# Kernel tuning notes

Hardware: AMD Instinct MI355X
Metric: run time of the kernel (lower is better)

## Reference

```python
import jax, jax.numpy as jnp
import numpy as np

EPS = 1e-6  # annotated-transformer LayerNorm eps


def setup_inputs() -> dict:
    key = jax.random.key(0)
    ks = jax.random.split(key, 6)
    B, S, D, F, G_dom = 32, 512, 1024, 2048, 4
    x = jax.random.normal(ks[0], (B, S, D), dtype=jnp.float32)
    # disjoint partition of the batch into 4 equal domain groups (like the
    # per-domain LongTensor index lists in the torch forward)
    perm = jax.random.permutation(ks[1], B).astype(jnp.int32)
    idx = perm.reshape(G_dom, B // G_dom)  # [4, 8]
    s1 = 1.0 / np.sqrt(D)
    s2 = 1.0 / np.sqrt(F)
    W1 = jax.random.normal(ks[2], (G_dom, D, F), dtype=jnp.float32) * s1
    B1 = jnp.zeros((G_dom, F), dtype=jnp.float32)
    W2 = jax.random.normal(ks[3], (G_dom, F, D), dtype=jnp.float32) * s2
    B2 = jnp.zeros((G_dom, D), dtype=jnp.float32)
    G = jnp.ones((G_dom, D), dtype=jnp.float32)
    Bn = jnp.zeros((G_dom, D), dtype=jnp.float32)
    return {"x": x, "idx": idx, "W1": W1, "B1": B1, "W2": W2, "B2": B2,
            "G": G, "Bn": Bn}


def _layer_norm(x, g, b):
    # matches torch: a_2 * (x - mean) / (std + eps) + b_2, std unbiased (ddof=1)
    mu = jnp.mean(x, axis=-1, keepdims=True)
    sd = jnp.std(x, axis=-1, keepdims=True, ddof=1)
    return g * (x - mu) / (sd + EPS) + b


def reference(x, idx, W1, B1, W2, B2, G, Bn):
    # gather per-domain token groups: [n_dom, per_dom, S, D]
    xg = x[idx]
    # SublayerConnection (eval mode, dropout off): x + adapter(norm(x))
    h = _layer_norm(xg, G[:, None, None, :], Bn[:, None, None, :])
    h = jax.nn.relu(jnp.einsum('gbsd,gdf->gbsf', h, W1) + B1[:, None, None, :])
    a = jnp.einsum('gbsf,gfd->gbsd', h, W2) + B2[:, None, None, :]
    out_g = xg + a
    # scatter combine (index_copy): indices are a disjoint partition
    S_, D_ = x.shape[1], x.shape[2]
    out = jnp.zeros_like(x).at[idx.reshape(-1)].set(out_g.reshape(-1, S_, D_))
    return out
```

## Files before the change

kernel.cpp:

```cpp
#include <hip/hip_runtime.h>
#include <hip/hip_bf16.h>


#define S_DIM 512
#define D_DIM 1024
#define F_DIM 2048
#define MPG   4096

typedef __attribute__((ext_vector_type(8))) short  short8;
typedef __attribute__((ext_vector_type(4))) float  f32x4;

__device__ __forceinline__ void gll16(const void* g, void* l) {
  __builtin_amdgcn_global_load_lds((__attribute__((address_space(1))) void*)g,
                                   (__attribute__((address_space(3))) void*)l,
                                   16, 0, 0);
}
#define VMC2()  asm volatile("s_waitcnt vmcnt(2)" ::: "memory")
#define VMC4()  asm volatile("s_waitcnt vmcnt(4)" ::: "memory")
#define SB()    __builtin_amdgcn_sched_barrier(0)
#define BAR()   __builtin_amdgcn_s_barrier()

__global__ __launch_bounds__(256) void transpose_cast_kernel(
    const float* __restrict__ W1, const float* __restrict__ W2,
    __hip_bfloat16* __restrict__ W1t, __hip_bfloat16* __restrict__ W2t)
{
  __shared__ float tl[32][33];
  const int bid = blockIdx.x;
  const float* src; __hip_bfloat16* dst;
  int R, C, tr, tc;
  if (bid < 8192) {
    const int g = bid >> 11, t = bid & 2047;
    R = 1024; C = 2048; tr = t >> 6; tc = t & 63;
    src = W1 + (size_t)g * R * C;
    dst = W1t + (size_t)g * R * C;
  } else {
    const int b2 = bid - 8192;
    const int g = b2 >> 11, t = b2 & 2047;
    R = 2048; C = 1024; tr = t >> 5; tc = t & 31;
    src = W2 + (size_t)g * R * C;
    dst = W2t + (size_t)g * R * C;
  }
  const int tx = threadIdx.x & 31, ty = threadIdx.x >> 5;
  const int r0 = tr * 32, c0 = tc * 32;
#pragma unroll
  for (int i = 0; i < 4; ++i)
    tl[ty + 8 * i][tx] = src[(size_t)(r0 + ty + 8 * i) * C + (c0 + tx)];
  __syncthreads();
#pragma unroll
  for (int i = 0; i < 4; ++i)
    dst[(size_t)(c0 + ty + 8 * i) * R + (r0 + tx)] = __float2bfloat16(tl[tx][ty + 8 * i]);
}

__global__ __launch_bounds__(256) void ln_gather_kernel(
    const float* __restrict__ x, const int* __restrict__ idx,
    const float* __restrict__ G, const float* __restrict__ Bn,
    __hip_bfloat16* __restrict__ Xn)
{
  const int wid  = (blockIdx.x * 256 + threadIdx.x) >> 6;
  const int lane = threadIdx.x & 63;
  const int g = wid >> 12;
  const int r = wid & 4095;
  const int j = r >> 9;
  const int tok = r & 511;
  const int b = idx[g * 8 + j];

  const float* src = x + ((size_t)b * S_DIM + tok) * D_DIM + lane * 16;
  float4 vq[4];
#pragma unroll
  for (int i = 0; i < 4; ++i) vq[i] = ((const float4*)src)[i];
  const float* va = (const float*)vq;

  float s = 0.f, s2 = 0.f;
#pragma unroll
  for (int i = 0; i < 16; ++i) { s += va[i]; s2 += va[i] * va[i]; }
#pragma unroll
  for (int o = 32; o > 0; o >>= 1) { s += __shfl_xor(s, o); s2 += __shfl_xor(s2, o); }

  const float mu  = s * (1.0f / 1024.0f);
  float var = fmaxf(s2 * (1.0f / 1024.0f) - mu * mu, 0.0f) * (1024.0f / 1023.0f);
  const float rs  = 1.0f / (sqrtf(var) + 1e-6f);

  float4 gq[4], bq[4];
  const float* gp = G  + (size_t)g * D_DIM + lane * 16;
  const float* bp = Bn + (size_t)g * D_DIM + lane * 16;
#pragma unroll
  for (int i = 0; i < 4; ++i) { gq[i] = ((const float4*)gp)[i]; bq[i] = ((const float4*)bp)[i]; }
  const float* ga = (const float*)gq;
  const float* be = (const float*)bq;

  __align__(16) __hip_bfloat16 ob[16];
#pragma unroll
  for (int i = 0; i < 16; ++i)
    ob[i] = __float2bfloat16(ga[i] * (va[i] - mu) * rs + be[i]);

  __hip_bfloat16* dst = Xn + ((size_t)g * MPG + r) * D_DIM + lane * 16;
  ((uint4*)dst)[0] = *(const uint4*)&ob[0];
  ((uint4*)dst)[1] = *(const uint4*)&ob[8];
}

template <bool SECOND>
__global__ __launch_bounds__(512, 2) void gemm_kernel(
    const __hip_bfloat16* __restrict__ A,
    const __hip_bfloat16* __restrict__ Bw,
    const float* __restrict__ bias,
    const float* __restrict__ xres,
    const int* __restrict__ idx,
    __hip_bfloat16* __restrict__ obf,
    float* __restrict__ of32,
    const int N, const int K, const int NT)
{
  extern __shared__ char lds[];
  const int ntile = N >> 8;
  const int nwg = gridDim.x;
  const int bid0 = blockIdx.x;
  const int bid = (bid0 & 7) * (nwg >> 3) + (bid0 >> 3);
  const int mt = bid / ntile, nt = bid % ntile;
  const int g  = mt >> 4;
  const int tid = threadIdx.x;
  const int w = tid >> 6, lane = tid & 63;
  const int wm = w >> 2, wn = w & 3;

  const __hip_bfloat16* Ab = A + (size_t)mt * 256 * K;
  const __hip_bfloat16* Bb = Bw + ((size_t)g * N + (size_t)nt * 256) * K;

  const int sp   = (lane & 7) ^ ((lane >> 3) & 7);
  const int srow = 2 * (lane >> 3) + (sp >> 2);
  const int skof = (sp & 3) * 8;
  const __hip_bfloat16* Ag0 = Ab + (size_t)(w * 32 + srow) * K + skof;
  const __hip_bfloat16* Ag1 = Ag0 + (size_t)16 * K;
  const __hip_bfloat16* Bg0 = Bb + (size_t)(w * 32 + srow) * K + skof;
  const __hip_bfloat16* Bg1 = Bg0 + (size_t)16 * K;

  const int l15 = lane & 15, sl = lane >> 4;
  const int slot_phys = (((l15 & 1) << 2) + sl) ^ ((l15 >> 1) & 7);
  const int lane_c = ((l15 >> 1) << 7) + (slot_phys << 4);

  f32x4 acc[8][4] = {};
  short8 frA0[4], frA1[4], frB0[4], frB1[4];

#define STAGE(BUFX, MAT, KH, TN) {                                          \
    const int koff = (TN) * 64 + (KH) * 32;                                 \
    char* d = lds + (BUFX) + ((KH) * 2 + (MAT)) * 16384 + w * 2048;         \
    if (MAT) { gll16(Bg0 + koff, d); gll16(Bg1 + koff, d + 1024); }         \
    else     { gll16(Ag0 + koff, d); gll16(Ag1 + koff, d + 1024); } }

#define RDA(DST, BUFX, KH, MH) {                                            \
    const char* base_ = lds + (BUFX) + (KH) * 32768 + wm * 8192 +           \
                        (MH) * 4096 + lane_c;                               \
    _Pragma("unroll") for (int mm = 0; mm < 4; ++mm)                        \
      DST[mm] = *(const short8*)(base_ + mm * 1024); }

#define RDB(DST, BUFX, KH) {                                                \
    const char* base_ = lds + (BUFX) + 16384 + (KH) * 32768 + wn * 4096 +   \
                        lane_c;                                             \
    _Pragma("unroll") for (int n = 0; n < 4; ++n)                           \
      DST[n] = *(const short8*)(base_ + n * 1024); }

#define MF(MH, FA, FB) {                                                    \
    __builtin_amdgcn_s_setprio(1);                                          \
    _Pragma("unroll") for (int mm = 0; mm < 4; ++mm)                        \
      _Pragma("unroll") for (int n = 0; n < 4; ++n)                         \
        acc[(MH) * 4 + mm][n] = __builtin_amdgcn_mfma_f32_16x16x32_bf16(    \
            FA[mm], FB[n], acc[(MH) * 4 + mm][n], 0, 0, 0);                 \
    __builtin_amdgcn_s_setprio(0); }

  STAGE(0, 0, 0, 0); STAGE(0, 1, 0, 0); STAGE(0, 0, 1, 0); STAGE(0, 1, 1, 0);
  VMC4();
  BAR();
  RDA(frA0, 0, 0, 0);
  RDB(frB0, 0, 0);

  for (int t = 0; t < NT; ++t) {
    const int bufb = (t & 1) << 16;
    const int bufx = bufb ^ 65536;
    const int tn = (t + 1 == NT) ? 0 : t + 1;
    SB(); BAR(); SB();
    RDA(frA1, bufb, 0, 1);
    STAGE(bufx, 0, 0, tn);
    SB();
    MF(0, frA0, frB0);
    SB(); VMC2(); BAR(); SB();
    RDA(frA0, bufb, 1, 0);
    RDB(frB1, bufb, 1);
    STAGE(bufx, 1, 0, tn);
    SB();
    MF(1, frA1, frB0);
    SB(); BAR(); SB();
    RDA(frA1, bufb, 1, 1);
    STAGE(bufx, 0, 1, tn);
    SB();
    MF(0, frA0, frB1);
    SB(); VMC2(); BAR(); SB();
    RDA(frA0, bufx, 0, 0);
    RDB(frB0, bufx, 0);
    STAGE(bufx, 1, 1, tn);
    SB();
    MF(1, frA1, frB1);
  }
#undef STAGE
#undef RDA
#undef RDB
#undef MF

  const int cc  = lane & 15;
  const int cr4 = (lane >> 4) * 4;

  float bv[4];
#pragma unroll
  for (int n = 0; n < 4; ++n)
    bv[n] = bias[(size_t)g * N + nt * 256 + wn * 64 + n * 16 + cc];

  if constexpr (!SECOND) {
#pragma unroll
    for (int m = 0; m < 8; ++m) {
      const int grow0 = mt * 256 + wm * 128 + m * 16 + cr4;
#pragma unroll
      for (int n = 0; n < 4; ++n) {
        const int gcol = nt * 256 + wn * 64 + n * 16 + cc;
#pragma unroll
        for (int i = 0; i < 4; ++i) {
          const float v = fmaxf(acc[m][n][i] + bv[n], 0.0f);
          obf[(size_t)(grow0 + i) * N + gcol] = __float2bfloat16(v);
        }
      }
    }
  } else {
    const int rbase = (mt & 15) * 256;
    const int b = idx[g * 8 + (rbase >> 9)];
    const size_t ob = (size_t)b * S_DIM * D_DIM;
#pragma unroll
    for (int m = 0; m < 8; ++m) {
      const int rloc = rbase + wm * 128 + m * 16 + cr4;
#pragma unroll
      for (int n = 0; n < 4; ++n) {
        const int gcol = nt * 256 + wn * 64 + n * 16 + cc;
#pragma unroll
        for (int i = 0; i < 4; ++i) {
          const int tok = (rloc + i) & 511;
          const size_t off = ob + (size_t)tok * D_DIM + gcol;
          of32[off] = acc[m][n][i] + bv[n] + xres[off];
        }
      }
    }
  }
}

extern "C" void kernel_launch(void* const* d_in, const int* in_sizes, int n_in,
                              void* d_out, int out_size, void* d_ws, size_t ws_size,
                              hipStream_t stream) {
  const float* x  = (const float*)d_in[0];
  const int*   idx = (const int*)d_in[1];
  const float* W1 = (const float*)d_in[2];
  const float* B1 = (const float*)d_in[3];
  const float* W2 = (const float*)d_in[4];
  const float* B2 = (const float*)d_in[5];
  const float* G  = (const float*)d_in[6];
  const float* Bn = (const float*)d_in[7];
  float* out = (float*)d_out;

  char* ws = (char*)d_ws;
  __hip_bfloat16* Xn  = (__hip_bfloat16*)(ws);
  __hip_bfloat16* W1t = (__hip_bfloat16*)(ws + 33554432);
  __hip_bfloat16* W2t = (__hip_bfloat16*)(ws + 50331648);
  __hip_bfloat16* H1  = (__hip_bfloat16*)(ws + 67108864);

  (void)hipFuncSetAttribute((const void*)gemm_kernel<false>,
                            hipFuncAttributeMaxDynamicSharedMemorySize, 131072);
  (void)hipFuncSetAttribute((const void*)gemm_kernel<true>,
                            hipFuncAttributeMaxDynamicSharedMemorySize, 131072);

  transpose_cast_kernel<<<dim3(16384), dim3(256), 0, stream>>>(W1, W2, W1t, W2t);
  ln_gather_kernel<<<dim3(4096), dim3(256), 0, stream>>>(x, idx, G, Bn, Xn);
  gemm_kernel<false><<<dim3(512), dim3(512), 131072, stream>>>(
      Xn, W1t, B1, nullptr, nullptr, H1, nullptr, F_DIM, D_DIM, 16);
  gemm_kernel<true><<<dim3(256), dim3(512), 131072, stream>>>(
      H1, W2t, B2, x, idx, nullptr, out, D_DIM, F_DIM, 32);
}
```

Measured before the change: 197.6 us.

## Replace double-buffered register fragments with single set and explicit LDS waits

Drops the ping-pong register fragments (frA0/frA1/frB0/frB1) for a single frA/frB set. Each MFMA block now waits on lgkmcnt(0) and barriers before and after, so LDS reads no longer overlap the previous block's MFMAs. This cuts VGPR pressure, which could allow higher occupancy. The cost is more barriers and serialized LDS-read/compute phases within a wave.

```diff
diff --git a/kernel.cpp b/kernel.cpp
--- a/kernel.cpp
+++ b/kernel.cpp
@@ -15,8 +15,8 @@
                                    (__attribute__((address_space(3))) void*)l,
                                    16, 0, 0);
 }
-#define VMC2()  asm volatile("s_waitcnt vmcnt(2)" ::: "memory")
 #define VMC4()  asm volatile("s_waitcnt vmcnt(4)" ::: "memory")
+#define LGKM0() asm volatile("s_waitcnt lgkmcnt(0)" ::: "memory")
 #define SB()    __builtin_amdgcn_sched_barrier(0)
 #define BAR()   __builtin_amdgcn_s_barrier()
 
@@ -136,7 +136,7 @@
   const int lane_c = ((l15 >> 1) << 7) + (slot_phys << 4);
 
   f32x4 acc[8][4] = {};
-  short8 frA0[4], frA1[4], frB0[4], frB1[4];
+  short8 frA[4], frB[4];
 
 #define STAGE(BUFX, MAT, KH, TN) {                                          \
     const int koff = (TN) * 64 + (KH) * 32;                                 \
@@ -144,58 +144,56 @@
     if (MAT) { gll16(Bg0 + koff, d); gll16(Bg1 + koff, d + 1024); }         \
     else     { gll16(Ag0 + koff, d); gll16(Ag1 + koff, d + 1024); } }
 
-#define RDA(DST, BUFX, KH, MH) {                                            \
+#define RDA(BUFX, KH, MH) {                                                 \
     const char* base_ = lds + (BUFX) + (KH) * 32768 + wm * 8192 +           \
                         (MH) * 4096 + lane_c;                               \
     _Pragma("unroll") for (int mm = 0; mm < 4; ++mm)                        \
-      DST[mm] = *(const short8*)(base_ + mm * 1024); }
-
-#define RDB(DST, BUFX, KH) {                                                \
+      frA[mm] = *(const short8*)(base_ + mm * 1024); }
+
+#define RDB(BUFX, KH) {                                                     \
     const char* base_ = lds + (BUFX) + 16384 + (KH) * 32768 + wn * 4096 +   \
                         lane_c;                                             \
     _Pragma("unroll") for (int n = 0; n < 4; ++n)                           \
-      DST[n] = *(const short8*)(base_ + n * 1024); }
-
-#define MF(MH, FA, FB) {                                                    \
+      frB[n] = *(const short8*)(base_ + n * 1024); }
+
+#define MF(MH) {                                                            \
     __builtin_amdgcn_s_setprio(1);                                          \
     _Pragma("unroll") for (int mm = 0; mm < 4; ++mm)                        \
       _Pragma("unroll") for (int n = 0; n < 4; ++n)                         \
         acc[(MH) * 4 + mm][n] = __builtin_amdgcn_mfma_f32_16x16x32_bf16(    \
-            FA[mm], FB[n], acc[(MH) * 4 + mm][n], 0, 0, 0);                 \
+            frA[mm], frB[n], acc[(MH) * 4 + mm][n], 0, 0, 0);               \
     __builtin_amdgcn_s_setprio(0); }
 
   STAGE(0, 0, 0, 0); STAGE(0, 1, 0, 0); STAGE(0, 0, 1, 0); STAGE(0, 1, 1, 0);
   VMC4();
   BAR();
-  RDA(frA0, 0, 0, 0);
-  RDB(frB0, 0, 0);
 
   for (int t = 0; t < NT; ++t) {
     const int bufb = (t & 1) << 16;
     const int bufx = bufb ^ 65536;
     const int tn = (t + 1 == NT) ? 0 : t + 1;
-    SB(); BAR(); SB();
-    RDA(frA1, bufb, 0, 1);
+    RDA(bufb, 0, 0); RDB(bufb, 0);
     STAGE(bufx, 0, 0, tn);
-    SB();
-    MF(0, frA0, frB0);
-    SB(); VMC2(); BAR(); SB();
-    RDA(frA0, bufb, 1, 0);
-    RDB(frB1, bufb, 1);
+    SB(); BAR(); LGKM0(); SB();
+    MF(0);
+    BAR();
+    RDA(bufb, 0, 1);
     STAGE(bufx, 1, 0, tn);
-    SB();
-    MF(1, frA1, frB0);
-    SB(); BAR(); SB();
-    RDA(frA1, bufb, 1, 1);
+    VMC4();
+    SB(); BAR(); LGKM0(); SB();
+    MF(1);
+    BAR();
+    RDA(bufb, 1, 0); RDB(bufb, 1);
     STAGE(bufx, 0, 1, tn);
-    SB();
-    MF(0, frA0, frB1);
-    SB(); VMC2(); BAR(); SB();
-    RDA(frA0, bufx, 0, 0);
-    RDB(frB0, bufx, 0);
+    SB(); BAR(); LGKM0(); SB();
+    MF(0);
+    BAR();
+    RDA(bufb, 1, 1);
     STAGE(bufx, 1, 1, tn);
-    SB();
-    MF(1, frA1, frB1);
+    VMC4();
+    SB(); BAR(); LGKM0(); SB();
+    MF(1);
+    BAR();
   }
 #undef STAGE
 #undef RDA
```

New measurement: 189.1 us. 1.05x faster.
